# Performance work log

Hardware: AMD Instinct MI355X
Metric: run time of the kernel (lower is better)

Reference implementation:

```python
import jax, jax.numpy as jnp
import numpy as np

N = 50000
E = 800000
IN_FEATS = 256
N_HIDDEN = 64
N_CLASSES = 40
HEADS = (4, 1)
NEG_SLOPE = 0.2  # DGL GATConv default


def gat_layer(x, src, dst, W, attn_l, attn_r, bias, n_heads, out_dim, activation):
    """One dglnn.GATConv layer (eval mode: dropout disabled).

    x: [N, F_in]; src/dst: [E] edge endpoints; W: [F_in, H*D];
    attn_l/attn_r: [H, D]; bias: [H*D]. Returns [N, H, D].
    """
    n = x.shape[0]
    z = (x @ W).reshape(n, n_heads, out_dim)            # [N, H, D]
    el = jnp.sum(z * attn_l[None], axis=-1)            # [N, H]
    er = jnp.sum(z * attn_r[None], axis=-1)            # [N, H]
    e = jax.nn.leaky_relu(el[src] + er[dst], NEG_SLOPE)  # [E, H]
    # segment softmax over incoming edges of each dst node
    m = jax.ops.segment_max(e, dst, num_segments=n)     # [N, H]
    a = jnp.exp(e - m[dst])                             # [E, H]
    s = jax.ops.segment_sum(a, dst, num_segments=n)     # [N, H]
    alpha = a / s[dst]                                  # [E, H]
    msg = alpha[:, :, None] * z[src]                    # [E, H, D]
    out = jax.ops.segment_sum(msg, dst, num_segments=n)  # [N, H, D]
    out = out + bias.reshape(1, n_heads, out_dim)
    if activation is not None:
        out = activation(out)
    return out


def setup_inputs() -> dict:
    key = jax.random.key(0)
    ks = jax.random.split(key, 12)
    H0, H1 = HEADS
    d_in1 = N_HIDDEN * H0
    def glorot(k, shape):
        fan = sum(shape[:2]) if len(shape) > 1 else shape[0]
        return jax.random.normal(k, shape, jnp.float32) * (2.0 / fan) ** 0.5
    return {
        "x": jax.random.normal(ks[0], (N, IN_FEATS), jnp.float32),
        "src": jax.random.randint(ks[1], (E,), 0, N),
        "dst": jax.random.randint(ks[2], (E,), 0, N),
        "W0": glorot(ks[3], (IN_FEATS, H0 * N_HIDDEN)),
        "attn_l0": glorot(ks[4], (H0, N_HIDDEN)),
        "attn_r0": glorot(ks[5], (H0, N_HIDDEN)),
        "bias0": jnp.zeros((H0 * N_HIDDEN,), jnp.float32),
        "W1": glorot(ks[6], (d_in1, H1 * N_CLASSES)),
        "attn_l1": glorot(ks[7], (H1, N_CLASSES)),
        "attn_r1": glorot(ks[8], (H1, N_CLASSES)),
        "bias1": jnp.zeros((H1 * N_CLASSES,), jnp.float32),
    }


def reference(x, src, dst, W0, attn_l0, attn_r0, bias0, W1, attn_l1, attn_r1, bias1):
    H0, H1 = HEADS
    # layer 0: GATConv + ELU, then flatten heads (l==0 branch)
    h = gat_layer(x, src, dst, W0, attn_l0, attn_r0, bias0,
                  H0, N_HIDDEN, jax.nn.elu)              # [N, H0, D]
    h = h.reshape(h.shape[0], -1)                        # [N, H0*D]
    # layer 1 (last): GATConv, no activation, head-mean (l==1 branch)
    h = gat_layer(h, src, dst, W1, attn_l1, attn_r1, bias1,
                  H1, N_CLASSES, None)                   # [N, H1, C]
    return h.mean(axis=1)                                # [N, C]
```

## Files before the change

kernel.cpp:

```cpp
#include <hip/hip_runtime.h>
#include <math.h>

using bf16x8 = __attribute__((ext_vector_type(8))) short;
using f32x4  = __attribute__((ext_vector_type(4))) float;

__device__ __forceinline__ unsigned short f2bf(float v) {
  unsigned int b = __float_as_uint(v);
  unsigned int r = (b + 0x7fffu + ((b >> 16) & 1u)) >> 16;
  return (unsigned short)r;
}
__device__ __forceinline__ float bf2f(unsigned short u) {
  return __uint_as_float(((unsigned int)u) << 16);
}


__global__ void pack_kernel(const float* __restrict__ W0f, unsigned short* __restrict__ Bp0,
                            const float* __restrict__ W1f, unsigned short* __restrict__ Bp1) {
  int idx = blockIdx.x * 256 + threadIdx.x;
  if (idx < 8192) {
    int lane = idx & 63, s = (idx >> 6) & 7, t = idx >> 9;
    int n = t * 16 + (lane & 15), quad = lane >> 4;
    unsigned short* o = Bp0 + (size_t)idx * 8;
    #pragma unroll
    for (int j = 0; j < 8; ++j) {
      int k = s * 32 + quad * 8 + j;
      o[j] = f2bf(W0f[(size_t)k * 256 + n]);
    }
  } else if (idx < 8192 + 1536) {
    int i1 = idx - 8192;
    int lane = i1 & 63, s = (i1 >> 6) & 7, t = i1 >> 9;
    int n = t * 16 + (lane & 15), quad = lane >> 4;
    unsigned short* o = Bp1 + (size_t)i1 * 8;
    #pragma unroll
    for (int j = 0; j < 8; ++j) {
      int k = s * 32 + quad * 8 + j;
      o[j] = (n < 40) ? f2bf(W1f[(size_t)k * 40 + n]) : 0;
    }
  }
}


__global__ void block_sum_kernel(const int* __restrict__ deg, int* __restrict__ bsum, int n) {
  __shared__ int red[4];
  int t = threadIdx.x, i = blockIdx.x * 256 + t;
  int v = (i < n) ? deg[i] : 0;
  #pragma unroll
  for (int off = 32; off; off >>= 1) v += __shfl_xor(v, off);
  if ((t & 63) == 0) red[t >> 6] = v;
  __syncthreads();
  if (t == 0) bsum[blockIdx.x] = red[0] + red[1] + red[2] + red[3];
}

__global__ void scan_bsum_kernel(const int* __restrict__ bsum, int* __restrict__ boffs,
                                 int* __restrict__ offsets, int nb, int n) {
  __shared__ int tmp[1024];
  int t = threadIdx.x;
  int v = (t < nb) ? bsum[t] : 0;
  tmp[t] = v;
  __syncthreads();
  #pragma unroll
  for (int off = 1; off < 1024; off <<= 1) {
    int add = (t >= off) ? tmp[t - off] : 0;
    __syncthreads();
    tmp[t] += add;
    __syncthreads();
  }
  if (t < nb) boffs[t] = tmp[t] - v;
  if (t == 1023) offsets[n] = tmp[1023];
}

__global__ void write_offsets_kernel(const int* __restrict__ deg, const int* __restrict__ boffs,
                                     int* __restrict__ offsets, int n) {
  __shared__ int tmp[256];
  int t = threadIdx.x, i = blockIdx.x * 256 + t;
  int v = (i < n) ? deg[i] : 0;
  tmp[t] = v;
  __syncthreads();
  #pragma unroll
  for (int off = 1; off < 256; off <<= 1) {
    int add = (t >= off) ? tmp[t - off] : 0;
    __syncthreads();
    tmp[t] += add;
    __syncthreads();
  }
  if (i < n) offsets[i] = boffs[blockIdx.x] + tmp[t] - v;
}


__global__ __launch_bounds__(512) void mega_hg_kernel(
    const float* __restrict__ A, const unsigned short* __restrict__ Bp,
    unsigned short* __restrict__ Zb,
    const float* __restrict__ al, const float* __restrict__ arr,
    float* __restrict__ el, float* __restrict__ er, int M,
    const int* __restrict__ dst, int* __restrict__ deg, int* __restrict__ slot,
    int E, int nG) {
  int bx = blockIdx.x;
  int tid = threadIdx.x;

  if (bx >= nG) {
    int t = (bx - nG) * 512 + tid;
    if (t < E) slot[t] = atomicAdd(&deg[dst[t]], 1);
    return;
  }

  int gx = bx >> 1, y = bx & 1;
  int wid = tid >> 6, lane = tid & 63;
  int quad = lane >> 4, col16 = lane & 15;
  int wr = wid >> 1, wc = wid & 1;
  int rowbase = gx * 256 + wr * 64;

  const float* aptr[4];
  #pragma unroll
  for (int rt = 0; rt < 4; ++rt) {
    int m = rowbase + rt * 16 + col16;
    if (m > M - 1) m = M - 1;
    aptr[rt] = A + (size_t)m * 256 + quad * 8;
  }

  f32x4 acc[4][4];
  #pragma unroll
  for (int rt = 0; rt < 4; ++rt)
    #pragma unroll
    for (int ct = 0; ct < 4; ++ct) acc[rt][ct] = {0.f, 0.f, 0.f, 0.f};

  const bf16x8* BpV = (const bf16x8*)Bp;

  auto loadA = [&](bf16x8* fr, int s) {
    #pragma unroll
    for (int rt = 0; rt < 4; ++rt) {
      const float* ap = aptr[rt] + s * 32;
      float4 a0 = *(const float4*)ap;
      float4 a1 = *(const float4*)(ap + 4);
      fr[rt][0] = (short)f2bf(a0.x); fr[rt][1] = (short)f2bf(a0.y);
      fr[rt][2] = (short)f2bf(a0.z); fr[rt][3] = (short)f2bf(a0.w);
      fr[rt][4] = (short)f2bf(a1.x); fr[rt][5] = (short)f2bf(a1.y);
      fr[rt][6] = (short)f2bf(a1.z); fr[rt][7] = (short)f2bf(a1.w);
    }
  };

  bf16x8 afc[4];
  loadA(afc, 0);
  for (int s = 0; s < 8; ++s) {
    bf16x8 afn[4];
    if (s < 7) loadA(afn, s + 1);
    #pragma unroll
    for (int ct = 0; ct < 4; ++ct) {
      bf16x8 bf = BpV[y * 4096 + ((wc * 4 + ct) * 8 + s) * 64 + lane];
      #pragma unroll
      for (int rt = 0; rt < 4; ++rt)
        acc[rt][ct] = __builtin_amdgcn_mfma_f32_16x16x32_bf16(afc[rt], bf, acc[rt][ct], 0, 0, 0);
    }
    if (s < 7) {
      #pragma unroll
      for (int rt = 0; rt < 4; ++rt) afc[rt] = afn[rt];
    }
  }

  int hw = y * 2 + wc;
  float al_c[4], ar_c[4];
  #pragma unroll
  for (int ct = 0; ct < 4; ++ct) {
    int col = y * 128 + (wc * 4 + ct) * 16 + col16;
    al_c[ct] = al[col];
    ar_c[ct] = arr[col];
  }

  #pragma unroll
  for (int rt = 0; rt < 4; ++rt) {
    int row0 = rowbase + rt * 16 + quad * 4;
    #pragma unroll
    for (int r = 0; r < 4; ++r) {
      int row = row0 + r;
      if (row < M) {
        #pragma unroll
        for (int ct = 0; ct < 4; ++ct) {
          int col = y * 128 + (wc * 4 + ct) * 16 + col16;
          Zb[(size_t)row * 256 + col] = f2bf(acc[rt][ct][r]);
        }
      }
      float pe = 0.f, pr = 0.f;
      #pragma unroll
      for (int ct = 0; ct < 4; ++ct) {
        float zv = acc[rt][ct][r];
        pe += zv * al_c[ct];
        pr += zv * ar_c[ct];
      }
      pe += __shfl_xor(pe, 1); pr += __shfl_xor(pr, 1);
      pe += __shfl_xor(pe, 2); pr += __shfl_xor(pr, 2);
      pe += __shfl_xor(pe, 4); pr += __shfl_xor(pr, 4);
      pe += __shfl_xor(pe, 8); pr += __shfl_xor(pr, 8);
      if (col16 == 0 && row < M) {
        el[(size_t)row * 4 + hw] = pe;
        er[(size_t)row * 4 + hw] = pr;
      }
    }
  }
}


__global__ __launch_bounds__(256) void csr_kernel(
    const int* __restrict__ src, const int* __restrict__ dst,
    const int* __restrict__ offs, const int* __restrict__ slot,
    int* __restrict__ ssrc, int E) {
  int e = blockIdx.x * 256 + threadIdx.x;
  if (e < E) {
    int p = offs[dst[e]] + slot[e];
    ssrc[p] = src[e];
  }
}


__global__ __launch_bounds__(256) void gemm1_mfma_kernel(
    const unsigned short* __restrict__ Ab, const unsigned short* __restrict__ Bp,
    unsigned short* __restrict__ Zb,
    const float* __restrict__ al, const float* __restrict__ arr,
    float* __restrict__ el, float* __restrict__ er, int M) {
  int wid = threadIdx.x >> 6, lane = threadIdx.x & 63;
  int quad = lane >> 4, col16 = lane & 15;
  int m = blockIdx.x * 64 + wid * 16 + col16;

  f32x4 acc[3];
  #pragma unroll
  for (int t = 0; t < 3; ++t) acc[t] = {0.f, 0.f, 0.f, 0.f};

  const bf16x8* BpV = (const bf16x8*)Bp;

  for (int s = 0; s < 8; ++s) {
    bf16x8 af;
    if (m < M) {
      af = *(const bf16x8*)(Ab + (size_t)m * 256 + s * 32 + quad * 8);
    } else {
      #pragma unroll
      for (int j = 0; j < 8; ++j) af[j] = 0;
    }
    #pragma unroll
    for (int t = 0; t < 3; ++t) {
      bf16x8 bf = BpV[(t * 8 + s) * 64 + lane];
      acc[t] = __builtin_amdgcn_mfma_f32_16x16x32_bf16(af, bf, acc[t], 0, 0, 0);
    }
  }

  float al_c[3], ar_c[3];
  #pragma unroll
  for (int t = 0; t < 3; ++t) {
    int col = t * 16 + col16;
    al_c[t] = (col < 40) ? al[col] : 0.f;
    ar_c[t] = (col < 40) ? arr[col] : 0.f;
  }

  int row0 = blockIdx.x * 64 + wid * 16 + quad * 4;
  #pragma unroll
  for (int r = 0; r < 4; ++r) {
    int row = row0 + r;
    if (row < M) {
      #pragma unroll
      for (int t = 0; t < 3; ++t) {
        int col = t * 16 + col16;
        if (col < 40) Zb[(size_t)row * 40 + col] = f2bf(acc[t][r]);
      }
    }
    float pe = 0.f, pr = 0.f;
    #pragma unroll
    for (int t = 0; t < 3; ++t) {
      pe += acc[t][r] * al_c[t];
      pr += acc[t][r] * ar_c[t];
    }
    pe += __shfl_xor(pe, 1); pr += __shfl_xor(pr, 1);
    pe += __shfl_xor(pe, 2); pr += __shfl_xor(pr, 2);
    pe += __shfl_xor(pe, 4); pr += __shfl_xor(pr, 4);
    pe += __shfl_xor(pe, 8); pr += __shfl_xor(pr, 8);
    if (col16 == 0 && row < M) {
      el[row] = pe;
      er[row] = pr;
    }
  }
}


__global__ __launch_bounds__(256) void agg0_kernel(
    const int* __restrict__ offs, const int* __restrict__ ssrc,
    const float* __restrict__ el, const float* __restrict__ er,
    const unsigned short* __restrict__ zb, const float* __restrict__ bias,
    unsigned short* __restrict__ outb, int n) {
  __shared__ float sW[4][16][4];
  __shared__ int   sS[4][16];
  int wid  = threadIdx.x >> 6;
  int lane = threadIdx.x & 63;
  int node = blockIdx.x * 4 + wid;
  if (node >= n) return;
  int c = lane & 3, eoff = lane >> 2;
  int half = lane >> 5, colg = lane & 31, h2 = colg >> 3;
  int s0 = offs[node], s1 = offs[node + 1];
  float er_c = er[node * 4 + c];
  const unsigned short* zcol = zb + (colg << 3);

  float ssum = 0.f;
  float acc[8] = {0.f, 0.f, 0.f, 0.f, 0.f, 0.f, 0.f, 0.f};
  for (int base = s0; base < s1; base += 16) {
    int cnt = min(16, s1 - base);
    if (eoff < cnt) {
      int esrc = ssrc[base + eoff];
      float v = el[esrc * 4 + c] + er_c;
      v = v > 0.f ? v : 0.2f * v;
      sW[wid][eoff][c] = expf(v);
      if (c == 0) sS[wid][eoff] = esrc;
    }
    for (int j = 0; j < cnt; j += 8) {
      float w[4];
      bf16x8 zu[4];
      #pragma unroll
      for (int u = 0; u < 4; ++u) {
        int jj = j + 2 * u + half;
        if (jj < cnt) {
          w[u] = sW[wid][jj][h2];
          int sn = sS[wid][jj];
          zu[u] = *(const bf16x8*)(zcol + (size_t)sn * 256);
        } else {
          w[u] = 0.f;
          #pragma unroll
          for (int i = 0; i < 8; ++i) zu[u][i] = 0;
        }
      }
      #pragma unroll
      for (int u = 0; u < 4; ++u) {
        ssum += w[u];
        #pragma unroll
        for (int i = 0; i < 8; ++i)
          acc[i] += w[u] * bf2f((unsigned short)zu[u][i]);
      }
    }
  }

  ssum += __shfl_xor(ssum, 32);
  #pragma unroll
  for (int i = 0; i < 8; ++i) acc[i] += __shfl_xor(acc[i], 32);

  float inv = (s1 > s0) ? 1.f / ssum : 0.f;
  if (half == 0) {
    const float4 b0v = *(const float4*)(bias + (colg << 3));
    const float4 b1v = *(const float4*)(bias + (colg << 3) + 4);
    float bb[8] = {b0v.x, b0v.y, b0v.z, b0v.w, b1v.x, b1v.y, b1v.z, b1v.w};
    bf16x8 u;
    #pragma unroll
    for (int i = 0; i < 8; ++i) {
      float o = acc[i] * inv + bb[i];
      o = o > 0.f ? o : expm1f(o);
      u[i] = (short)f2bf(o);
    }
    *(bf16x8*)(outb + (size_t)node * 256 + (colg << 3)) = u;
  }
}


__global__ __launch_bounds__(256) void agg1_kernel(
    const int* __restrict__ offs, const int* __restrict__ ssrc,
    const float* __restrict__ el, const float* __restrict__ er,
    const unsigned short* __restrict__ zb, const float* __restrict__ bias,
    float* __restrict__ out, int n) {
  __shared__ float sW[4][64];
  __shared__ int   sS[4][64];
  int wid  = threadIdx.x >> 6;
  int lane = threadIdx.x & 63;
  int node = blockIdx.x * 4 + wid;
  if (node >= n) return;
  int half = lane >> 5, d = lane & 31;
  int s0 = offs[node], s1 = offs[node + 1];
  float ern = er[node];

  float ssum = 0.f;
  float2 acc = make_float2(0.f, 0.f);
  for (int base = s0; base < s1; base += 64) {
    int cnt = min(64, s1 - base);
    if (lane < cnt) {
      int esrc = ssrc[base + lane];
      float v = el[esrc] + ern;
      v = v > 0.f ? v : 0.2f * v;
      sW[wid][lane] = expf(v);
      sS[wid][lane] = esrc;
    }
    for (int j = 0; j < cnt; j += 2) {
      int jj = j + half;
      float w = (jj < cnt) ? sW[wid][jj] : 0.f;
      int sn = sS[wid][(jj < cnt) ? jj : (cnt - 1)];
      ssum += w;
      if (d < 20) {
        unsigned zp = *(const unsigned*)(zb + (size_t)sn * 40 + (d << 1));
        acc.x += w * bf2f((unsigned short)(zp & 0xffffu));
        acc.y += w * bf2f((unsigned short)(zp >> 16));
      }
    }
  }

  ssum  += __shfl_xor(ssum, 32);
  acc.x += __shfl_xor(acc.x, 32);
  acc.y += __shfl_xor(acc.y, 32);

  float inv = (s1 > s0) ? 1.f / ssum : 0.f;
  if (half == 0 && d < 20) {
    float2 o;
    o.x = acc.x * inv + bias[(d << 1) + 0];
    o.y = acc.y * inv + bias[(d << 1) + 1];
    *(float2*)(out + (size_t)node * 40 + (d << 1)) = o;
  }
}


extern "C" void kernel_launch(void* const* d_in, const int* in_sizes, int n_in,
                              void* d_out, int out_size, void* d_ws, size_t ws_size,
                              hipStream_t stream) {
  const float* x   = (const float*)d_in[0];
  const int*   src = (const int*)d_in[1];
  const int*   dst = (const int*)d_in[2];
  const float* W0  = (const float*)d_in[3];
  const float* al0 = (const float*)d_in[4];
  const float* ar0 = (const float*)d_in[5];
  const float* b0  = (const float*)d_in[6];
  const float* W1  = (const float*)d_in[7];
  const float* al1 = (const float*)d_in[8];
  const float* ar1 = (const float*)d_in[9];
  const float* b1  = (const float*)d_in[10];
  float* out = (float*)d_out;

  const int N = in_sizes[0] / 256;
  const int E = in_sizes[1];
  const int NB = (N + 255) / 256;

  char* ws = (char*)d_ws;
  size_t off = 0;
  auto alloc = [&](size_t bytes) {
    void* p = ws + off;
    off = (off + bytes + 255) & ~(size_t)255;
    return p;
  };
  unsigned short* z0b = (unsigned short*)alloc((size_t)N * 256 * 2);
  unsigned short* h0b = (unsigned short*)alloc((size_t)N * 256 * 2);
  unsigned short* z1b = (unsigned short*)alloc((size_t)N * 40 * 2);
  unsigned short* w0p = (unsigned short*)alloc((size_t)16 * 8 * 64 * 8 * 2);
  unsigned short* w1p = (unsigned short*)alloc((size_t)3 * 8 * 64 * 8 * 2);
  float* el0  = (float*)alloc((size_t)N * 4 * 4);
  float* er0  = (float*)alloc((size_t)N * 4 * 4);
  float* el1  = (float*)alloc((size_t)N * 4);
  float* er1  = (float*)alloc((size_t)N * 4);
  int* deg    = (int*)alloc((size_t)N * 4);
  int* offs   = (int*)alloc((size_t)(N + 1) * 4);
  int* slot   = (int*)alloc((size_t)E * 4);
  int* bsum   = (int*)alloc((size_t)NB * 4);
  int* boffs  = (int*)alloc((size_t)NB * 4);
  int* ssrc   = (int*)alloc((size_t)E * 4);
  (void)off; (void)ws_size; (void)n_in; (void)out_size;

  const int nG = ((N + 255) / 256) * 2;
  const int nH512 = (E + 511) / 512;
  const int nCSR = (E + 255) / 256;

  hipMemsetAsync(deg, 0, (size_t)N * 4, stream);
  pack_kernel<<<38, 256, 0, stream>>>(W0, w0p, W1, w1p);
  mega_hg_kernel<<<nG + nH512, 512, 0, stream>>>(x, w0p, z0b, al0, ar0, el0, er0, N,
                                                 dst, deg, slot, E, nG);
  block_sum_kernel<<<NB, 256, 0, stream>>>(deg, bsum, N);
  scan_bsum_kernel<<<1, 1024, 0, stream>>>(bsum, boffs, offs, NB, N);
  write_offsets_kernel<<<NB, 256, 0, stream>>>(deg, boffs, offs, N);
  csr_kernel<<<nCSR, 256, 0, stream>>>(src, dst, offs, slot, ssrc, E);
  agg0_kernel<<<(N + 3) / 4, 256, 0, stream>>>(offs, ssrc, el0, er0, z0b, b0, h0b, N);
  gemm1_mfma_kernel<<<(N + 63) / 64, 256, 0, stream>>>(h0b, w1p, z1b, al1, ar1, el1, er1, N);
  agg1_kernel<<<(N + 3) / 4, 256, 0, stream>>>(offs, ssrc, el1, er1, z1b, b1, out, N);
}
```

Measured before the change: 302.5 us.

## Fuse layer-1 projection and attention logits into layer-0 aggregation epilogue

Removes the separate MFMA GEMM for layer 1 and the bf16 h0 intermediate buffer. Each wave now computes its node's 256-wide ELU output in registers and immediately takes 40 fp32 dot products against a transposed W1, using shuffle reductions, then writes z1 and el1/er1. This saves an N×256 bf16 write and re-read plus one kernel launch. In exchange it swaps tensor-core matmul for scalar FMAs with many cross-lane shuffles in the aggregation kernel.

```diff
diff --git a/kernel.cpp b/kernel.cpp
--- a/kernel.cpp
+++ b/kernel.cpp
@@ -15,7 +15,7 @@
 
 
 __global__ void pack_kernel(const float* __restrict__ W0f, unsigned short* __restrict__ Bp0,
-                            const float* __restrict__ W1f, unsigned short* __restrict__ Bp1) {
+                            const float* __restrict__ W1f, float* __restrict__ W1T) {
   int idx = blockIdx.x * 256 + threadIdx.x;
   if (idx < 8192) {
     int lane = idx & 63, s = (idx >> 6) & 7, t = idx >> 9;
@@ -26,15 +26,13 @@
       int k = s * 32 + quad * 8 + j;
       o[j] = f2bf(W0f[(size_t)k * 256 + n]);
     }
-  } else if (idx < 8192 + 1536) {
+  } else if (idx < 8192 + 1280) {
     int i1 = idx - 8192;
-    int lane = i1 & 63, s = (i1 >> 6) & 7, t = i1 >> 9;
-    int n = t * 16 + (lane & 15), quad = lane >> 4;
-    unsigned short* o = Bp1 + (size_t)i1 * 8;
     #pragma unroll
     for (int j = 0; j < 8; ++j) {
-      int k = s * 32 + quad * 8 + j;
-      o[j] = (n < 40) ? f2bf(W1f[(size_t)k * 40 + n]) : 0;
+      int l = i1 * 8 + j;
+      int c = l >> 8, k = l & 255;
+      W1T[l] = W1f[(size_t)k * 40 + c];
     }
   }
 }
@@ -210,78 +208,14 @@
 }
 
 
-__global__ __launch_bounds__(256) void gemm1_mfma_kernel(
-    const unsigned short* __restrict__ Ab, const unsigned short* __restrict__ Bp,
-    unsigned short* __restrict__ Zb,
-    const float* __restrict__ al, const float* __restrict__ arr,
-    float* __restrict__ el, float* __restrict__ er, int M) {
-  int wid = threadIdx.x >> 6, lane = threadIdx.x & 63;
-  int quad = lane >> 4, col16 = lane & 15;
-  int m = blockIdx.x * 64 + wid * 16 + col16;
-
-  f32x4 acc[3];
-  #pragma unroll
-  for (int t = 0; t < 3; ++t) acc[t] = {0.f, 0.f, 0.f, 0.f};
-
-  const bf16x8* BpV = (const bf16x8*)Bp;
-
-  for (int s = 0; s < 8; ++s) {
-    bf16x8 af;
-    if (m < M) {
-      af = *(const bf16x8*)(Ab + (size_t)m * 256 + s * 32 + quad * 8);
-    } else {
-      #pragma unroll
-      for (int j = 0; j < 8; ++j) af[j] = 0;
-    }
-    #pragma unroll
-    for (int t = 0; t < 3; ++t) {
-      bf16x8 bf = BpV[(t * 8 + s) * 64 + lane];
-      acc[t] = __builtin_amdgcn_mfma_f32_16x16x32_bf16(af, bf, acc[t], 0, 0, 0);
-    }
-  }
-
-  float al_c[3], ar_c[3];
-  #pragma unroll
-  for (int t = 0; t < 3; ++t) {
-    int col = t * 16 + col16;
-    al_c[t] = (col < 40) ? al[col] : 0.f;
-    ar_c[t] = (col < 40) ? arr[col] : 0.f;
-  }
-
-  int row0 = blockIdx.x * 64 + wid * 16 + quad * 4;
-  #pragma unroll
-  for (int r = 0; r < 4; ++r) {
-    int row = row0 + r;
-    if (row < M) {
-      #pragma unroll
-      for (int t = 0; t < 3; ++t) {
-        int col = t * 16 + col16;
-        if (col < 40) Zb[(size_t)row * 40 + col] = f2bf(acc[t][r]);
-      }
-    }
-    float pe = 0.f, pr = 0.f;
-    #pragma unroll
-    for (int t = 0; t < 3; ++t) {
-      pe += acc[t][r] * al_c[t];
-      pr += acc[t][r] * ar_c[t];
-    }
-    pe += __shfl_xor(pe, 1); pr += __shfl_xor(pr, 1);
-    pe += __shfl_xor(pe, 2); pr += __shfl_xor(pr, 2);
-    pe += __shfl_xor(pe, 4); pr += __shfl_xor(pr, 4);
-    pe += __shfl_xor(pe, 8); pr += __shfl_xor(pr, 8);
-    if (col16 == 0 && row < M) {
-      el[row] = pe;
-      er[row] = pr;
-    }
-  }
-}
-
-
-__global__ __launch_bounds__(256) void agg0_kernel(
+__global__ __launch_bounds__(256) void agg0_fused_kernel(
     const int* __restrict__ offs, const int* __restrict__ ssrc,
     const float* __restrict__ el, const float* __restrict__ er,
     const unsigned short* __restrict__ zb, const float* __restrict__ bias,
-    unsigned short* __restrict__ outb, int n) {
+    const float* __restrict__ W1T, const float* __restrict__ al1,
+    const float* __restrict__ ar1,
+    unsigned short* __restrict__ z1b, float* __restrict__ el1,
+    float* __restrict__ er1, int n) {
   __shared__ float sW[4][16][4];
   __shared__ int   sS[4][16];
   int wid  = threadIdx.x >> 6;
@@ -336,18 +270,38 @@
   for (int i = 0; i < 8; ++i) acc[i] += __shfl_xor(acc[i], 32);
 
   float inv = (s1 > s0) ? 1.f / ssum : 0.f;
-  if (half == 0) {
-    const float4 b0v = *(const float4*)(bias + (colg << 3));
-    const float4 b1v = *(const float4*)(bias + (colg << 3) + 4);
-    float bb[8] = {b0v.x, b0v.y, b0v.z, b0v.w, b1v.x, b1v.y, b1v.z, b1v.w};
-    bf16x8 u;
-    #pragma unroll
-    for (int i = 0; i < 8; ++i) {
-      float o = acc[i] * inv + bb[i];
-      o = o > 0.f ? o : expm1f(o);
-      u[i] = (short)f2bf(o);
-    }
-    *(bf16x8*)(outb + (size_t)node * 256 + (colg << 3)) = u;
+  const float4 b0v = *(const float4*)(bias + (colg << 3));
+  const float4 b1v = *(const float4*)(bias + (colg << 3) + 4);
+  float bb[8] = {b0v.x, b0v.y, b0v.z, b0v.w, b1v.x, b1v.y, b1v.z, b1v.w};
+  float h0v[8];
+  #pragma unroll
+  for (int i = 0; i < 8; ++i) {
+    float o = acc[i] * inv + bb[i];
+    h0v[i] = o > 0.f ? o : expm1f(o);
+  }
+
+  float el1a = 0.f, er1a = 0.f;
+  #pragma unroll
+  for (int j = 0; j < 20; ++j) {
+    int cc = half * 20 + j;
+    const float* wc = W1T + (size_t)cc * 256 + (colg << 3);
+    float4 w0 = *(const float4*)wc;
+    float4 w1 = *(const float4*)(wc + 4);
+    float d = h0v[0] * w0.x + h0v[1] * w0.y + h0v[2] * w0.z + h0v[3] * w0.w
+            + h0v[4] * w1.x + h0v[5] * w1.y + h0v[6] * w1.z + h0v[7] * w1.w;
+    d += __shfl_xor(d, 1);  d += __shfl_xor(d, 2);  d += __shfl_xor(d, 4);
+    d += __shfl_xor(d, 8);  d += __shfl_xor(d, 16);
+    if (colg == 0) {
+      z1b[(size_t)node * 40 + cc] = f2bf(d);
+      el1a += d * al1[cc];
+      er1a += d * ar1[cc];
+    }
+  }
+  el1a += __shfl_xor(el1a, 32);
+  er1a += __shfl_xor(er1a, 32);
+  if (lane == 0) {
+    el1[node] = el1a;
+    er1[node] = er1a;
   }
 }
 
@@ -433,10 +387,9 @@
     return p;
   };
   unsigned short* z0b = (unsigned short*)alloc((size_t)N * 256 * 2);
-  unsigned short* h0b = (unsigned short*)alloc((size_t)N * 256 * 2);
   unsigned short* z1b = (unsigned short*)alloc((size_t)N * 40 * 2);
   unsigned short* w0p = (unsigned short*)alloc((size_t)16 * 8 * 64 * 8 * 2);
-  unsigned short* w1p = (unsigned short*)alloc((size_t)3 * 8 * 64 * 8 * 2);
+  float* w1t  = (float*)alloc((size_t)40 * 256 * 4);
   float* el0  = (float*)alloc((size_t)N * 4 * 4);
   float* er0  = (float*)alloc((size_t)N * 4 * 4);
   float* el1  = (float*)alloc((size_t)N * 4);
@@ -454,14 +407,14 @@
   const int nCSR = (E + 255) / 256;
 
   hipMemsetAsync(deg, 0, (size_t)N * 4, stream);
-  pack_kernel<<<38, 256, 0, stream>>>(W0, w0p, W1, w1p);
+  pack_kernel<<<37, 256, 0, stream>>>(W0, w0p, W1, w1t);
   mega_hg_kernel<<<nG + nH512, 512, 0, stream>>>(x, w0p, z0b, al0, ar0, el0, er0, N,
                                                  dst, deg, slot, E, nG);
   block_sum_kernel<<<NB, 256, 0, stream>>>(deg, bsum, N);
   scan_bsum_kernel<<<1, 1024, 0, stream>>>(bsum, boffs, offs, NB, N);
   write_offsets_kernel<<<NB, 256, 0, stream>>>(deg, boffs, offs, N);
   csr_kernel<<<nCSR, 256, 0, stream>>>(src, dst, offs, slot, ssrc, E);
-  agg0_kernel<<<(N + 3) / 4, 256, 0, stream>>>(offs, ssrc, el0, er0, z0b, b0, h0b, N);
-  gemm1_mfma_kernel<<<(N + 63) / 64, 256, 0, stream>>>(h0b, w1p, z1b, al1, ar1, el1, er1, N);
+  agg0_fused_kernel<<<(N + 3) / 4, 256, 0, stream>>>(offs, ssrc, el0, er0, z0b, b0,
+                                                     w1t, al1, ar1, z1b, el1, er1, N);
   agg1_kernel<<<(N + 3) / 4, 256, 0, stream>>>(offs, ssrc, el1, er1, z1b, b1, out, N);
 }
```

Result: slower. 359.4 us (+18.8%).

## Fuse degree scan and CSR scatter into one cooperative kernel

Applied to the files above, without the earlier changes.

Replaces the four separate launches (block sum, scan of block sums, offset write, CSR scatter) with a single cooperative kernel that separates the phases with grid-wide syncs. The aim is to remove the launch gaps and tail effects between those small kernels. The scan of block sums assumes at most 256 chunks, which holds for N=50000 (196 chunks), and the old four-kernel path is kept as a fallback if the cooperative launch fails. Grid syncs add their own cost, and the grid is fixed at 1024 blocks.

```diff
diff --git a/kernel.cpp b/kernel.cpp
--- a/kernel.cpp
+++ b/kernel.cpp
@@ -1,5 +1,8 @@
 #include <hip/hip_runtime.h>
+#include <hip/hip_cooperative_groups.h>
 #include <math.h>
+
+namespace cg = cooperative_groups;
 
 using bf16x8 = __attribute__((ext_vector_type(8))) short;
 using f32x4  = __attribute__((ext_vector_type(4))) float;
@@ -84,6 +87,75 @@
     __syncthreads();
   }
   if (i < n) offsets[i] = boffs[blockIdx.x] + tmp[t] - v;
+}
+
+__global__ __launch_bounds__(256) void csr_kernel(
+    const int* __restrict__ src, const int* __restrict__ dst,
+    const int* __restrict__ offs, const int* __restrict__ slot,
+    int* __restrict__ ssrc, int E) {
+  int e = blockIdx.x * 256 + threadIdx.x;
+  if (e < E) {
+    int p = offs[dst[e]] + slot[e];
+    ssrc[p] = src[e];
+  }
+}
+
+
+__global__ __launch_bounds__(256) void scan_csr_kernel(
+    const int* __restrict__ src, const int* __restrict__ dst,
+    const int* __restrict__ deg, int* __restrict__ bsum, int* __restrict__ boffs,
+    int* __restrict__ offs, const int* __restrict__ slot,
+    int* __restrict__ ssrc, int E, int n, int nCh) {
+  cg::grid_group grid = cg::this_grid();
+  __shared__ int tmp[256];
+  int bx = blockIdx.x, t = threadIdx.x;
+
+  if (bx < nCh) {
+    int i = bx * 256 + t;
+    int v = (i < n) ? deg[i] : 0;
+    int s = v;
+    #pragma unroll
+    for (int off = 32; off; off >>= 1) s += __shfl_xor(s, off);
+    if ((t & 63) == 0) tmp[t >> 6] = s;
+    __syncthreads();
+    if (t == 0) bsum[bx] = tmp[0] + tmp[1] + tmp[2] + tmp[3];
+  }
+  grid.sync();
+
+  if (bx == 0) {
+    int v = (t < nCh) ? bsum[t] : 0;
+    tmp[t] = v;
+    __syncthreads();
+    for (int off = 1; off < 256; off <<= 1) {
+      int a = (t >= off) ? tmp[t - off] : 0;
+      __syncthreads();
+      tmp[t] += a;
+      __syncthreads();
+    }
+    if (t < nCh) boffs[t] = tmp[t] - v;
+    if (t == 255) offs[n] = tmp[255];
+  }
+  grid.sync();
+
+  if (bx < nCh) {
+    int i = bx * 256 + t;
+    int v = (i < n) ? deg[i] : 0;
+    tmp[t] = v;
+    __syncthreads();
+    for (int off = 1; off < 256; off <<= 1) {
+      int a = (t >= off) ? tmp[t - off] : 0;
+      __syncthreads();
+      tmp[t] += a;
+      __syncthreads();
+    }
+    if (i < n) offs[i] = boffs[bx] + tmp[t] - v;
+  }
+  grid.sync();
+
+  for (int e = bx * 256 + t; e < E; e += gridDim.x * 256) {
+    int p = offs[dst[e]] + slot[e];
+    ssrc[p] = src[e];
+  }
 }
 
 
@@ -194,18 +266,6 @@
         er[(size_t)row * 4 + hw] = pr;
       }
     }
-  }
-}
-
-
-__global__ __launch_bounds__(256) void csr_kernel(
-    const int* __restrict__ src, const int* __restrict__ dst,
-    const int* __restrict__ offs, const int* __restrict__ slot,
-    int* __restrict__ ssrc, int E) {
-  int e = blockIdx.x * 256 + threadIdx.x;
-  if (e < E) {
-    int p = offs[dst[e]] + slot[e];
-    ssrc[p] = src[e];
   }
 }
 
@@ -457,10 +517,22 @@
   pack_kernel<<<38, 256, 0, stream>>>(W0, w0p, W1, w1p);
   mega_hg_kernel<<<nG + nH512, 512, 0, stream>>>(x, w0p, z0b, al0, ar0, el0, er0, N,
                                                  dst, deg, slot, E, nG);
-  block_sum_kernel<<<NB, 256, 0, stream>>>(deg, bsum, N);
-  scan_bsum_kernel<<<1, 1024, 0, stream>>>(bsum, boffs, offs, NB, N);
-  write_offsets_kernel<<<NB, 256, 0, stream>>>(deg, boffs, offs, N);
-  csr_kernel<<<nCSR, 256, 0, stream>>>(src, dst, offs, slot, ssrc, E);
+  {
+    int Ev = E, Nv = N, nChv = NB;
+    const int* srcv = src; const int* dstv = dst; const int* degv = deg;
+    const int* slotv = slot;
+    void* kargs[] = {(void*)&srcv, (void*)&dstv, (void*)&degv, (void*)&bsum,
+                     (void*)&boffs, (void*)&offs, (void*)&slotv, (void*)&ssrc,
+                     (void*)&Ev, (void*)&Nv, (void*)&nChv};
+    hipError_t rc = hipLaunchCooperativeKernel((const void*)scan_csr_kernel,
+                                               dim3(1024), dim3(256), kargs, 0, stream);
+    if (rc != hipSuccess) {
+      block_sum_kernel<<<NB, 256, 0, stream>>>(deg, bsum, N);
+      scan_bsum_kernel<<<1, 1024, 0, stream>>>(bsum, boffs, offs, NB, N);
+      write_offsets_kernel<<<NB, 256, 0, stream>>>(deg, boffs, offs, N);
+      csr_kernel<<<nCSR, 256, 0, stream>>>(src, dst, offs, slot, ssrc, E);
+    }
+  }
   agg0_kernel<<<(N + 3) / 4, 256, 0, stream>>>(offs, ssrc, el0, er0, z0b, b0, h0b, N);
   gemm1_mfma_kernel<<<(N + 63) / 64, 256, 0, stream>>>(h0b, w1p, z1b, al1, ar1, el1, er1, N);
   agg1_kernel<<<(N + 3) / 4, 256, 0, stream>>>(offs, ssrc, el1, er1, z1b, b1, out, N);
```

Result: slower. 645.5 us (+113.4%).
